# Performance work log

Measured on AMD Instinct MI355X. Metric: run time of the kernel, lower is better.

## Reference

```python
import jax, jax.numpy as jnp
import numpy as np

LOW_THRESH = 0.3
HIGH_THRESH = 0.7
BATCH_SIZE = 256
NUM_POS = BATCH_SIZE // 2   # 128; guaranteed <= total_pos since B2=512 GT boxes are scattered positive
NUM_NEG = BATCH_SIZE - NUM_POS


def _xcycwh_to_x1y1x2y2(b):
    xc, yc, w, h = b[..., 0], b[..., 1], b[..., 2], b[..., 3]
    return jnp.stack([xc - w / 2, yc - h / 2, xc + w / 2, yc + h / 2], axis=-1)


def box_iou(box1, box2):
    # box1: (1, B1, 4), box2: (1, B2, 4) in (xc, yc, w, h) -> iou (1, B1, B2)
    area1 = box1[..., 2] * box1[..., 3]              # (1, B1)
    area2 = box2[..., 2] * box2[..., 3]              # (1, B2)
    c1 = _xcycwh_to_x1y1x2y2(box1)[:, :, None, :]    # (1, B1, 1, 4)
    c2 = _xcycwh_to_x1y1x2y2(box2)[:, None, :, :]    # (1, 1, B2, 4)
    x0 = jnp.maximum(c1[..., 0], c2[..., 0])
    y0 = jnp.maximum(c1[..., 1], c2[..., 1])
    x1 = jnp.minimum(c1[..., 2], c2[..., 2])
    y1 = jnp.minimum(c1[..., 3], c2[..., 3])
    inter = jnp.maximum(x1 - x0, 0.0) * jnp.maximum(y1 - y0, 0.0)  # (1, B1, B2)
    return inter / (area1[:, :, None] + area2[:, None, :] - inter)


def setup_inputs() -> dict:
    key = jax.random.key(0)
    k1, k2, k3, k4 = jax.random.split(key, 4)
    return {
        "input_boxes": jax.random.uniform(k1, (1, 50000, 4), dtype=jnp.float32),
        "target_boxes": jax.random.uniform(k2, (1, 512, 4), dtype=jnp.float32),
        "pos_noise": jax.random.uniform(k3, (50000,), dtype=jnp.float32),
        "neg_noise": jax.random.uniform(k4, (50000,), dtype=jnp.float32),
    }


def reference(input_boxes, target_boxes, pos_noise, neg_noise):
    ious = box_iou(input_boxes, target_boxes)        # (1, B1, B2)
    input_max_iou = jnp.max(ious, axis=2)            # (1, B1) best GT per proposal
    input_idx = jnp.argmax(ious, axis=2)             # (1, B1)
    target_idx = jnp.argmax(ious, axis=1)            # (1, B2) best proposal per GT

    pos_mask = input_max_iou[0] > HIGH_THRESH        # (B1,)
    neg_mask = input_max_iou[0] < LOW_THRESH
    # each GT's best-matching proposal is forced positive (scatter_)
    pos_mask = pos_mask.at[target_idx[0]].set(True)
    neg_mask = neg_mask.at[target_idx[0]].set(False)
    # fallback: if no negatives at all, negatives = complement of positives
    neg_mask = jnp.where(jnp.sum(neg_mask) == 0, ~pos_mask, neg_mask)

    # uniform sampling without replacement == top-k over iid uniform noise restricted to the mask
    pos_scores = jnp.where(pos_mask, pos_noise, -1.0)
    _, pos_input_idx = jax.lax.top_k(pos_scores, NUM_POS)      # (NUM_POS,)
    neg_scores = jnp.where(neg_mask, neg_noise, -1.0)
    _, neg_input_idx = jax.lax.top_k(neg_scores, NUM_NEG)      # (NUM_NEG,)

    pos_target_idx = input_idx[0][pos_input_idx]               # (NUM_POS,)
    return pos_input_idx, pos_target_idx, neg_input_idx
```

## Files before the change

### kernel.cpp

```cpp
#include <hip/hip_runtime.h>
#include <stdint.h>

#pragma clang fp contract(off)

typedef unsigned long long ull;

#define HIGHT 0.7f
#define LOWT  0.3f
#define KSEL  128
#define CAP   2048
#define MAXGT 512
#define TPB   256
#define CHUNK 32
#define TJ    128
#define SMP   132
#define NLAD  7

__device__ __constant__ float LADV[NLAD] = {0.998f, 0.99f, 0.95f, 0.8f, 0.5f, 0.25f, 0.0625f};

__device__ __forceinline__ float iou_pair(float ax0, float ay0, float ax1, float ay1, float aarea,
                                          float bx0, float by0, float bx1, float by1, float barea){
#pragma clang fp contract(off)
  float x0 = fmaxf(ax0, bx0);
  float y0 = fmaxf(ay0, by0);
  float x1 = fminf(ax1, bx1);
  float y1 = fminf(ay1, by1);
  float dx = fmaxf(x1 - x0, 0.0f);
  float dy = fmaxf(y1 - y0, 0.0f);
  float inter = dx * dy;
  float uni = (aarea + barea) - inter;
  return inter / uni;
}

__global__ __launch_bounds__(TPB)
void fused_iou(const float4* __restrict__ boxes, const float4* __restrict__ gts,
               int n1, int n2, int nblk,
               float* __restrict__ max_iou, int* __restrict__ input_idx,
               ull* __restrict__ colpart, int* __restrict__ forced,
               int* __restrict__ cnts_part, int* __restrict__ cnts,
               const float* __restrict__ pn, const float* __restrict__ nn)
{
#pragma clang fp contract(off)
  const int b = blockIdx.x, t = threadIdx.x;

  for (int x = b * TPB + t; x < n1; x += nblk * TPB) forced[x] = 0;
  if (b == 0 && t < 32) cnts[t] = 0;

  __shared__ float4 gc[MAXGT];
  __shared__ float  ga[MAXGT];
  __shared__ float  smat[CHUNK * SMP];
  __shared__ float  sm[CHUNK];

  for (int j = t; j < n2; j += TPB){
    float4 g = gts[j];
    float hw = g.z * 0.5f, hh = g.w * 0.5f;
    gc[j] = make_float4(g.x - hw, g.y - hh, g.x + hw, g.y + hh);
    ga[j] = g.z * g.w;
  }
  __syncthreads();

  const int lo = b * CHUNK;
  int cr = n1 - lo; if (cr > CHUNK) cr = CHUNK; if (cr < 0) cr = 0;

  const int pi = t >> 3, q = t & 7;
  const bool valid = (pi < cr);
  float px0 = 0, py0 = 0, px1 = 0, py1 = 0, pa = 0;
  if (valid){
    float4 pb = boxes[lo + pi];
    float hw = pb.z * 0.5f, hh = pb.w * 0.5f;
    px0 = pb.x - hw; py0 = pb.y - hh; px1 = pb.x + hw; py1 = pb.y + hh;
    pa = pb.z * pb.w;
  }
  float vA = -1.0f, vB = -1.0f; int jA = 0, jB = 0;

  for (int tb = 0; tb < n2; tb += TJ){
    const int tn = min(TJ, n2 - tb);
    if (valid){
      const int jlim = tb + tn;
      int s = 0;
      for (;; s += 2){
        int j0 = tb + q + 8 * s;
        int j1 = j0 + 8;
        if (j1 < jlim){
          float4 g0 = gc[j0]; float a0 = ga[j0];
          float4 g1 = gc[j1]; float a1 = ga[j1];
          float u = iou_pair(px0, py0, px1, py1, pa, g0.x, g0.y, g0.z, g0.w, a0);
          float w = iou_pair(px0, py0, px1, py1, pa, g1.x, g1.y, g1.z, g1.w, a1);
          smat[pi * SMP + (j0 - tb)] = u;
          smat[pi * SMP + (j1 - tb)] = w;
          if (u > vA){ vA = u; jA = j0; }
          if (w > vB){ vB = w; jB = j1; }
        } else {
          if (j0 < jlim){
            float4 g0 = gc[j0]; float a0 = ga[j0];
            float u = iou_pair(px0, py0, px1, py1, pa, g0.x, g0.y, g0.z, g0.w, a0);
            smat[pi * SMP + (j0 - tb)] = u;
            if (u > vA){ vA = u; jA = j0; }
          }
          break;
        }
      }
    }
    __syncthreads();
    {
      const int jloc = t >> 1, half = t & 1;
      if (jloc < tn){
        float cv = -1.0f; int cp = 0;
        const int p0 = half * 16;
        const int p1 = min(p0 + 16, cr);
        for (int p = p0; p < p1; ++p){
          float v = smat[p * SMP + jloc];
          if (v > cv){ cv = v; cp = p; }
        }
        float ov = __shfl_xor(cv, 1, 64);
        int   op = __shfl_xor(cp, 1, 64);
        if (ov > cv || (ov == cv && op < cp)){ cv = ov; cp = op; }
        if (half == 0){
          colpart[(size_t)b * n2 + (tb + jloc)] =
            ((ull)__float_as_uint(cv) << 32) | (ull)(unsigned)~(unsigned)(lo + cp);
        }
      }
    }
    __syncthreads();
  }

  if (vB > vA || (vB == vA && jB < jA)){ vA = vB; jA = jB; }
  #pragma unroll
  for (int m = 1; m <= 4; m <<= 1){
    float ov = __shfl_xor(vA, m, 64);
    int   oj = __shfl_xor(jA, m, 64);
    if (ov > vA || (ov == vA && oj < jA)){ vA = ov; jA = oj; }
  }
  if (valid && q == 0){
    max_iou[lo + pi] = vA;
    input_idx[lo + pi] = jA;
    sm[pi] = vA;
  }
  __syncthreads();

  if (t < 64){
    const bool vld = (t < cr);
    float m = vld ? sm[t] : -1.0f;
    bool pos = vld && (m > HIGHT);
    bool nm  = vld && (m < LOWT);
    bool np  = vld && !(m > HIGHT);
    float sp = pos ? pn[lo + t] : -1.0f;
    float sn = (nm || np) ? nn[lo + t] : -1.0f;
    int c[24];
    c[0] = __popcll(__ballot(pos));
    c[1] = __popcll(__ballot(nm));
    c[2] = __popcll(__ballot(np));
    #pragma unroll
    for (int k = 0; k < NLAD; ++k){
      float L = LADV[k];
      c[3 + k]  = __popcll(__ballot(pos && sp > L));
      c[10 + k] = __popcll(__ballot(nm  && sn > L));
      c[17 + k] = __popcll(__ballot(np  && sn > L));
    }
    if (t == 0){
      #pragma unroll
      for (int k = 0; k < 24; ++k) cnts_part[b * 24 + k] = c[k];
    }
  }
}

__global__ __launch_bounds__(TPB)
void colfix_kernel(const ull* __restrict__ colpart, int n1, int n2, int nblk,
                   const float* __restrict__ max_iou,
                   const float* __restrict__ pn, const float* __restrict__ nn,
                   int* __restrict__ forced, const int* __restrict__ cnts_part,
                   int* __restrict__ cnts)
{
  const int t = threadIdx.x;
  __shared__ ull red[TPB];
  __shared__ int ired[TPB];

  if (blockIdx.x < (unsigned)n2){
    const int jj = blockIdx.x;
    ull m = 0;
    for (int x = t; x < nblk; x += TPB){
      ull v = colpart[(size_t)x * n2 + jj];
      if (v > m) m = v;
    }
    red[t] = m;
    __syncthreads();
    for (int s = TPB >> 1; s > 0; s >>= 1){
      if (t < s && red[t + s] > red[t]) red[t] = red[t + s];
      __syncthreads();
    }
    if (t == 0){
      unsigned idx = ~(unsigned)(red[0] & 0xFFFFFFFFull);
      if (idx < (unsigned)n1){
        int old = atomicExch(&forced[idx], 1);
        if (old == 0){
          float m2 = max_iou[idx];
          if (!(m2 > HIGHT)){
            float sp = pn[idx];
            float sn = nn[idx];
            atomicAdd(&cnts[0], 1);
            atomicAdd(&cnts[2], -1);
            #pragma unroll
            for (int k = 0; k < NLAD; ++k){
              float L = LADV[k];
              if (sp > L) atomicAdd(&cnts[3 + k], 1);
              if (sn > L) atomicAdd(&cnts[17 + k], -1);
            }
            if (m2 < LOWT){
              atomicAdd(&cnts[1], -1);
              #pragma unroll
              for (int k = 0; k < NLAD; ++k)
                if (sn > LADV[k]) atomicAdd(&cnts[10 + k], -1);
            }
          }
        }
      }
    }
  } else {
    const int k = blockIdx.x - n2;
    int s = 0;
    for (int x = t; x < nblk; x += TPB) s += cnts_part[x * 24 + k];
    ired[t] = s;
    __syncthreads();
    for (int st = TPB >> 1; st > 0; st >>= 1){
      if (t < st) ired[t] += ired[t + st];
      __syncthreads();
    }
    if (t == 0 && ired[0]) atomicAdd(&cnts[k], ired[0]);
  }
}

__device__ __forceinline__ float pick_tau(const int* lad, int tot){
  if (tot <= CAP) return -1.0f;
  for (int k = 0; k < NLAD; ++k)
    if (lad[k] >= KSEL) return LADV[k];
  return -1.0f;
}

__global__ __launch_bounds__(TPB)
void collect_kernel(const float* __restrict__ max_iou, const int* __restrict__ forced,
                    const float* __restrict__ pn, const float* __restrict__ nn,
                    int n1, int* __restrict__ cnts, ull* __restrict__ cand)
{
  __shared__ int s_c[24];
  const int t = threadIdx.x;
  if (t < 24) s_c[t] = cnts[t];
  __syncthreads();
  const bool fb = (s_c[1] == 0);
  const int totP = s_c[0];
  const int totN = fb ? s_c[2] : s_c[1];
  const float tauP = pick_tau(&s_c[3], totP);
  const float tauN = pick_tau(fb ? &s_c[17] : &s_c[10], totN);

  const int i = blockIdx.x * TPB + t;
  if (i >= n1) return;
  float m = max_iou[i];
  bool f = forced[i] != 0;
  bool pos = (m > HIGHT) || f;
  if (pos){
    float sc = pn[i];
    if (sc > tauP){
      int p = atomicAdd(&cnts[24], 1);
      if (p < CAP) cand[p] = ((ull)(__float_as_uint(sc) + 1u) << 32) | (ull)(unsigned)~(unsigned)i;
    }
  } else if (totP < KSEL && i < 2 * KSEL){
    int p = atomicAdd(&cnts[24], 1);
    if (p < CAP) cand[p] = (ull)(unsigned)~(unsigned)i;
  }
  bool seln = fb ? (!pos) : ((m < LOWT) && !f);
  if (seln){
    float sc = nn[i];
    if (sc > tauN){
      int p = atomicAdd(&cnts[25], 1);
      if (p < CAP) cand[CAP + p] = ((ull)(__float_as_uint(sc) + 1u) << 32) | (ull)(unsigned)~(unsigned)i;
    }
  } else if (totN < KSEL && i < 2 * KSEL){
    int p = atomicAdd(&cnts[25], 1);
    if (p < CAP) cand[CAP + p] = (ull)(unsigned)~(unsigned)i;
  }
}

__global__ __launch_bounds__(1024)
void select_kernel(const ull* __restrict__ cand, const int* __restrict__ cnts,
                   const int* __restrict__ input_idx, int* __restrict__ out)
{
  const int t = threadIdx.x;
  const bool isPos = (blockIdx.x == 0);
  __shared__ ull keys[CAP];
  int n = cnts[isPos ? 24 : 25]; if (n > CAP) n = CAP;
  for (int x = t; x < n; x += 1024)
    keys[x] = cand[(isPos ? 0 : CAP) + x];
  __syncthreads();
  ull mk[2]; int mr[2]; int ne = 0;
  for (int x = t; x < n; x += 1024){ mk[ne] = keys[x]; mr[ne] = 0; ++ne; }
  for (int o = 0; o < n; ++o){
    ull ko = keys[o];
    if (ne > 0) mr[0] += (ko > mk[0]);
    if (ne > 1) mr[1] += (ko > mk[1]);
  }
  for (int e = 0; e < ne; ++e){
    int r = mr[e];
    if (r < KSEL){
      unsigned idx = ~(unsigned)(mk[e] & 0xFFFFFFFFull);
      if (isPos){ out[r] = (int)idx; out[KSEL + r] = input_idx[idx]; }
      else        out[2 * KSEL + r] = (int)idx;
    }
  }
}

extern "C" void kernel_launch(void* const* d_in, const int* in_sizes, int n_in,
                              void* d_out, int out_size, void* d_ws, size_t ws_size,
                              hipStream_t stream){
  const float4* boxes = (const float4*)d_in[0];
  const float4* gts   = (const float4*)d_in[1];
  const float* pos_noise = (const float*)d_in[2];
  const float* neg_noise = (const float*)d_in[3];
  const int n1 = in_sizes[0] / 4;
  const int n2 = in_sizes[1] / 4;
  int* out = (int*)d_out;

  char* ws = (char*)d_ws;
  size_t off = 0;
  auto carve = [&](size_t bytes) -> char* {
    char* p = ws + off;
    off = (off + bytes + 255) & ~(size_t)255;
    return p;
  };
  const int nblk = (n1 + CHUNK - 1) / CHUNK;
  float* max_iou   = (float*)carve((size_t)n1 * 4);
  int*   input_idx = (int*)  carve((size_t)n1 * 4);
  ull*   colpart   = (ull*)  carve((size_t)nblk * n2 * 8);
  int*   forced    = (int*)  carve((size_t)n1 * 4);
  int*   cnts_part = (int*)  carve((size_t)nblk * 24 * 4);
  int*   cnts      = (int*)  carve(32 * 4);
  ull*   cand      = (ull*)  carve((size_t)2 * CAP * 8);

  const int gb = (n1 + TPB - 1) / TPB;
  fused_iou<<<nblk, TPB, 0, stream>>>(boxes, gts, n1, n2, nblk,
                                      max_iou, input_idx, colpart, forced,
                                      cnts_part, cnts, pos_noise, neg_noise);
  colfix_kernel<<<n2 + 24, TPB, 0, stream>>>(colpart, n1, n2, nblk, max_iou,
                                             pos_noise, neg_noise, forced, cnts_part, cnts);
  collect_kernel<<<gb, TPB, 0, stream>>>(max_iou, forced, pos_noise, neg_noise,
                                         n1, cnts, cand);
  select_kernel<<<2, 1024, 0, stream>>>(cand, cnts, input_idx, out);
}
```

Measured before the change: 137.3 us.

## Replace per-block column partials with global atomicMax and atomic count accumulation

Result: slower. 297.2 us (+116.4%).

```diff
diff --git a/kernel.cpp b/kernel.cpp
--- a/kernel.cpp
+++ b/kernel.cpp
@@ -32,19 +32,27 @@
   return inter / uni;
 }
 
+__global__ __launch_bounds__(256)
+void zero_init(ull* __restrict__ colmax, int* __restrict__ cnts)
+{
+  const int t = threadIdx.x;
+  colmax[t] = 0;
+  colmax[t + 256] = 0;
+  if (t < 32) cnts[t] = 0;
+}
+
 __global__ __launch_bounds__(TPB)
 void fused_iou(const float4* __restrict__ boxes, const float4* __restrict__ gts,
                int n1, int n2, int nblk,
                float* __restrict__ max_iou, int* __restrict__ input_idx,
-               ull* __restrict__ colpart, int* __restrict__ forced,
-               int* __restrict__ cnts_part, int* __restrict__ cnts,
+               ull* __restrict__ colmax, int* __restrict__ forced,
+               int* __restrict__ cnts,
                const float* __restrict__ pn, const float* __restrict__ nn)
 {
 #pragma clang fp contract(off)
   const int b = blockIdx.x, t = threadIdx.x;
 
   for (int x = b * TPB + t; x < n1; x += nblk * TPB) forced[x] = 0;
-  if (b == 0 && t < 32) cnts[t] = 0;
 
   __shared__ float4 gc[MAXGT];
   __shared__ float  ga[MAXGT];
@@ -116,8 +124,8 @@
         int   op = __shfl_xor(cp, 1, 64);
         if (ov > cv || (ov == cv && op < cp)){ cv = ov; cp = op; }
         if (half == 0){
-          colpart[(size_t)b * n2 + (tb + jloc)] =
-            ((ull)__float_as_uint(cv) << 32) | (ull)(unsigned)~(unsigned)(lo + cp);
+          ull key = ((ull)__float_as_uint(cv) << 32) | (ull)(unsigned)~(unsigned)(lo + cp);
+          atomicMax(&colmax[tb + jloc], key);
         }
       }
     }
@@ -159,73 +167,41 @@
     }
     if (t == 0){
       #pragma unroll
-      for (int k = 0; k < 24; ++k) cnts_part[b * 24 + k] = c[k];
-    }
-  }
-}
-
-__global__ __launch_bounds__(TPB)
-void colfix_kernel(const ull* __restrict__ colpart, int n1, int n2, int nblk,
-                   const float* __restrict__ max_iou,
-                   const float* __restrict__ pn, const float* __restrict__ nn,
-                   int* __restrict__ forced, const int* __restrict__ cnts_part,
-                   int* __restrict__ cnts)
+      for (int k = 0; k < 24; ++k) if (c[k]) atomicAdd(&cnts[k], c[k]);
+    }
+  }
+}
+
+__global__ __launch_bounds__(512)
+void forcefix(const ull* __restrict__ colmax, int n1, int n2,
+              const float* __restrict__ max_iou,
+              const float* __restrict__ pn, const float* __restrict__ nn,
+              int* __restrict__ forced, int* __restrict__ cnts)
 {
   const int t = threadIdx.x;
-  __shared__ ull red[TPB];
-  __shared__ int ired[TPB];
-
-  if (blockIdx.x < (unsigned)n2){
-    const int jj = blockIdx.x;
-    ull m = 0;
-    for (int x = t; x < nblk; x += TPB){
-      ull v = colpart[(size_t)x * n2 + jj];
-      if (v > m) m = v;
-    }
-    red[t] = m;
-    __syncthreads();
-    for (int s = TPB >> 1; s > 0; s >>= 1){
-      if (t < s && red[t + s] > red[t]) red[t] = red[t + s];
-      __syncthreads();
-    }
-    if (t == 0){
-      unsigned idx = ~(unsigned)(red[0] & 0xFFFFFFFFull);
-      if (idx < (unsigned)n1){
-        int old = atomicExch(&forced[idx], 1);
-        if (old == 0){
-          float m2 = max_iou[idx];
-          if (!(m2 > HIGHT)){
-            float sp = pn[idx];
-            float sn = nn[idx];
-            atomicAdd(&cnts[0], 1);
-            atomicAdd(&cnts[2], -1);
-            #pragma unroll
-            for (int k = 0; k < NLAD; ++k){
-              float L = LADV[k];
-              if (sp > L) atomicAdd(&cnts[3 + k], 1);
-              if (sn > L) atomicAdd(&cnts[17 + k], -1);
-            }
-            if (m2 < LOWT){
-              atomicAdd(&cnts[1], -1);
-              #pragma unroll
-              for (int k = 0; k < NLAD; ++k)
-                if (sn > LADV[k]) atomicAdd(&cnts[10 + k], -1);
-            }
-          }
-        }
-      }
-    }
-  } else {
-    const int k = blockIdx.x - n2;
-    int s = 0;
-    for (int x = t; x < nblk; x += TPB) s += cnts_part[x * 24 + k];
-    ired[t] = s;
-    __syncthreads();
-    for (int st = TPB >> 1; st > 0; st >>= 1){
-      if (t < st) ired[t] += ired[t + st];
-      __syncthreads();
-    }
-    if (t == 0 && ired[0]) atomicAdd(&cnts[k], ired[0]);
+  if (t >= n2) return;
+  ull key = colmax[t];
+  unsigned idx = ~(unsigned)(key & 0xFFFFFFFFull);
+  if (idx >= (unsigned)n1) return;
+  int old = atomicExch(&forced[idx], 1);
+  if (old != 0) return;
+  float m2 = max_iou[idx];
+  if (m2 > HIGHT) return;
+  float sp = pn[idx];
+  float sn = nn[idx];
+  atomicAdd(&cnts[0], 1);
+  atomicAdd(&cnts[2], -1);
+  #pragma unroll
+  for (int k = 0; k < NLAD; ++k){
+    float L = LADV[k];
+    if (sp > L) atomicAdd(&cnts[3 + k], 1);
+    if (sn > L) atomicAdd(&cnts[17 + k], -1);
+  }
+  if (m2 < LOWT){
+    atomicAdd(&cnts[1], -1);
+    #pragma unroll
+    for (int k = 0; k < NLAD; ++k)
+      if (sn > LADV[k]) atomicAdd(&cnts[10 + k], -1);
   }
 }
 
@@ -328,18 +304,18 @@
   const int nblk = (n1 + CHUNK - 1) / CHUNK;
   float* max_iou   = (float*)carve((size_t)n1 * 4);
   int*   input_idx = (int*)  carve((size_t)n1 * 4);
-  ull*   colpart   = (ull*)  carve((size_t)nblk * n2 * 8);
   int*   forced    = (int*)  carve((size_t)n1 * 4);
-  int*   cnts_part = (int*)  carve((size_t)nblk * 24 * 4);
+  ull*   colmax    = (ull*)  carve((size_t)MAXGT * 8);
   int*   cnts      = (int*)  carve(32 * 4);
   ull*   cand      = (ull*)  carve((size_t)2 * CAP * 8);
 
   const int gb = (n1 + TPB - 1) / TPB;
+  zero_init<<<1, 256, 0, stream>>>(colmax, cnts);
   fused_iou<<<nblk, TPB, 0, stream>>>(boxes, gts, n1, n2, nblk,
-                                      max_iou, input_idx, colpart, forced,
-                                      cnts_part, cnts, pos_noise, neg_noise);
-  colfix_kernel<<<n2 + 24, TPB, 0, stream>>>(colpart, n1, n2, nblk, max_iou,
-                                             pos_noise, neg_noise, forced, cnts_part, cnts);
+                                      max_iou, input_idx, colmax, forced,
+                                      cnts, pos_noise, neg_noise);
+  forcefix<<<1, 512, 0, stream>>>(colmax, n1, n2, max_iou,
+                                  pos_noise, neg_noise, forced, cnts);
   collect_kernel<<<gb, TPB, 0, stream>>>(max_iou, forced, pos_noise, neg_noise,
                                          n1, cnts, cand);
   select_kernel<<<2, 1024, 0, stream>>>(cand, cnts, input_idx, out);
```

## Replace per-column reduction blocks with coalesced grid reduction and last-block fixup

Applied to the files above, without the earlier changes.

Result: slower. 151.5 us (+10.4%).

```diff
diff --git a/kernel.cpp b/kernel.cpp
--- a/kernel.cpp
+++ b/kernel.cpp
@@ -15,6 +15,7 @@
 #define TJ    128
 #define SMP   132
 #define NLAD  7
+#define RB    64
 
 __device__ __constant__ float LADV[NLAD] = {0.998f, 0.99f, 0.95f, 0.8f, 0.5f, 0.25f, 0.0625f};
 
@@ -38,13 +39,17 @@
                float* __restrict__ max_iou, int* __restrict__ input_idx,
                ull* __restrict__ colpart, int* __restrict__ forced,
                int* __restrict__ cnts_part, int* __restrict__ cnts,
+               ull* __restrict__ colmax,
                const float* __restrict__ pn, const float* __restrict__ nn)
 {
 #pragma clang fp contract(off)
   const int b = blockIdx.x, t = threadIdx.x;
 
   for (int x = b * TPB + t; x < n1; x += nblk * TPB) forced[x] = 0;
-  if (b == 0 && t < 32) cnts[t] = 0;
+  if (b == 0){
+    if (t < 32) cnts[t] = 0;
+    for (int x = t; x < n2; x += TPB) colmax[x] = 0;
+  }
 
   __shared__ float4 gc[MAXGT];
   __shared__ float  ga[MAXGT];
@@ -71,34 +76,38 @@
     px0 = pb.x - hw; py0 = pb.y - hh; px1 = pb.x + hw; py1 = pb.y + hh;
     pa = pb.z * pb.w;
   }
-  float vA = -1.0f, vB = -1.0f; int jA = 0, jB = 0;
+  float vA = -1.0f, vB = -1.0f, vC = -1.0f, vD = -1.0f;
+  int jA = 0, jB = 0, jC = 0, jD = 0;
 
   for (int tb = 0; tb < n2; tb += TJ){
     const int tn = min(TJ, n2 - tb);
     if (valid){
       const int jlim = tb + tn;
-      int s = 0;
-      for (;; s += 2){
-        int j0 = tb + q + 8 * s;
-        int j1 = j0 + 8;
-        if (j1 < jlim){
-          float4 g0 = gc[j0]; float a0 = ga[j0];
-          float4 g1 = gc[j1]; float a1 = ga[j1];
-          float u = iou_pair(px0, py0, px1, py1, pa, g0.x, g0.y, g0.z, g0.w, a0);
-          float w = iou_pair(px0, py0, px1, py1, pa, g1.x, g1.y, g1.z, g1.w, a1);
-          smat[pi * SMP + (j0 - tb)] = u;
-          smat[pi * SMP + (j1 - tb)] = w;
-          if (u > vA){ vA = u; jA = j0; }
-          if (w > vB){ vB = w; jB = j1; }
-        } else {
-          if (j0 < jlim){
-            float4 g0 = gc[j0]; float a0 = ga[j0];
-            float u = iou_pair(px0, py0, px1, py1, pa, g0.x, g0.y, g0.z, g0.w, a0);
-            smat[pi * SMP + (j0 - tb)] = u;
-            if (u > vA){ vA = u; jA = j0; }
-          }
-          break;
-        }
+      int j0 = tb + q;
+      for (; j0 + 24 < jlim; j0 += 32){
+        const int ja = j0, jb = j0 + 8, jc = j0 + 16, jd = j0 + 24;
+        float4 gA = gc[ja]; float aA = ga[ja];
+        float4 gB = gc[jb]; float aB = ga[jb];
+        float4 gC = gc[jc]; float aC = ga[jc];
+        float4 gD = gc[jd]; float aD = ga[jd];
+        float u = iou_pair(px0, py0, px1, py1, pa, gA.x, gA.y, gA.z, gA.w, aA);
+        float v = iou_pair(px0, py0, px1, py1, pa, gB.x, gB.y, gB.z, gB.w, aB);
+        float w = iou_pair(px0, py0, px1, py1, pa, gC.x, gC.y, gC.z, gC.w, aC);
+        float x = iou_pair(px0, py0, px1, py1, pa, gD.x, gD.y, gD.z, gD.w, aD);
+        smat[pi * SMP + (ja - tb)] = u;
+        smat[pi * SMP + (jb - tb)] = v;
+        smat[pi * SMP + (jc - tb)] = w;
+        smat[pi * SMP + (jd - tb)] = x;
+        if (u > vA){ vA = u; jA = ja; }
+        if (v > vB){ vB = v; jB = jb; }
+        if (w > vC){ vC = w; jC = jc; }
+        if (x > vD){ vD = x; jD = jd; }
+      }
+      for (; j0 < jlim; j0 += 8){
+        float4 g0 = gc[j0]; float a0 = ga[j0];
+        float u = iou_pair(px0, py0, px1, py1, pa, g0.x, g0.y, g0.z, g0.w, a0);
+        smat[pi * SMP + (j0 - tb)] = u;
+        if (u > vA){ vA = u; jA = j0; }
       }
     }
     __syncthreads();
@@ -125,6 +134,8 @@
   }
 
   if (vB > vA || (vB == vA && jB < jA)){ vA = vB; jA = jB; }
+  if (vC > vA || (vC == vA && jC < jA)){ vA = vC; jA = jC; }
+  if (vD > vA || (vD == vA && jD < jA)){ vA = vD; jA = jD; }
   #pragma unroll
   for (int m = 1; m <= 4; m <<= 1){
     float ov = __shfl_xor(vA, m, 64);
@@ -164,68 +175,63 @@
   }
 }
 
-__global__ __launch_bounds__(TPB)
-void colfix_kernel(const ull* __restrict__ colpart, int n1, int n2, int nblk,
-                   const float* __restrict__ max_iou,
-                   const float* __restrict__ pn, const float* __restrict__ nn,
-                   int* __restrict__ forced, const int* __restrict__ cnts_part,
-                   int* __restrict__ cnts)
+__global__ __launch_bounds__(256)
+void colreduce(const ull* __restrict__ colpart, int n1, int n2, int nblk,
+               const float* __restrict__ max_iou,
+               const float* __restrict__ pn, const float* __restrict__ nn,
+               int* __restrict__ forced, const int* __restrict__ cnts_part,
+               int* __restrict__ cnts, ull* __restrict__ colmax)
 {
-  const int t = threadIdx.x;
-  __shared__ ull red[TPB];
-  __shared__ int ired[TPB];
-
-  if (blockIdx.x < (unsigned)n2){
-    const int jj = blockIdx.x;
+  const int t = threadIdx.x, b = blockIdx.x, nb = gridDim.x;
+
+  for (int j = t; j < n2; j += 256){
     ull m = 0;
-    for (int x = t; x < nblk; x += TPB){
-      ull v = colpart[(size_t)x * n2 + jj];
+    for (int x = b; x < nblk; x += nb){
+      ull v = colpart[(size_t)x * n2 + j];
       if (v > m) m = v;
     }
-    red[t] = m;
-    __syncthreads();
-    for (int s = TPB >> 1; s > 0; s >>= 1){
-      if (t < s && red[t + s] > red[t]) red[t] = red[t + s];
-      __syncthreads();
-    }
-    if (t == 0){
-      unsigned idx = ~(unsigned)(red[0] & 0xFFFFFFFFull);
-      if (idx < (unsigned)n1){
-        int old = atomicExch(&forced[idx], 1);
-        if (old == 0){
-          float m2 = max_iou[idx];
-          if (!(m2 > HIGHT)){
-            float sp = pn[idx];
-            float sn = nn[idx];
-            atomicAdd(&cnts[0], 1);
-            atomicAdd(&cnts[2], -1);
+    if (m) atomicMax(&colmax[j], m);
+  }
+  if (t < 24){
+    int s = 0;
+    for (int x = b; x < nblk; x += nb) s += cnts_part[x * 24 + t];
+    if (s) atomicAdd(&cnts[t], s);
+  }
+
+  __threadfence();
+  __shared__ int islast;
+  if (t == 0) islast = (atomicAdd(&cnts[26], 1) == nb - 1) ? 1 : 0;
+  __syncthreads();
+  if (!islast) return;
+  __threadfence();
+
+  for (int j = t; j < n2; j += 256){
+    ull key = __hip_atomic_load(&colmax[j], __ATOMIC_RELAXED, __HIP_MEMORY_SCOPE_AGENT);
+    unsigned idx = ~(unsigned)(key & 0xFFFFFFFFull);
+    if (idx < (unsigned)n1){
+      int old = atomicExch(&forced[idx], 1);
+      if (old == 0){
+        float m2 = max_iou[idx];
+        if (!(m2 > HIGHT)){
+          float sp = pn[idx];
+          float sn = nn[idx];
+          atomicAdd(&cnts[0], 1);
+          atomicAdd(&cnts[2], -1);
+          #pragma unroll
+          for (int k = 0; k < NLAD; ++k){
+            float L = LADV[k];
+            if (sp > L) atomicAdd(&cnts[3 + k], 1);
+            if (sn > L) atomicAdd(&cnts[17 + k], -1);
+          }
+          if (m2 < LOWT){
+            atomicAdd(&cnts[1], -1);
             #pragma unroll
-            for (int k = 0; k < NLAD; ++k){
-              float L = LADV[k];
-              if (sp > L) atomicAdd(&cnts[3 + k], 1);
-              if (sn > L) atomicAdd(&cnts[17 + k], -1);
-            }
-            if (m2 < LOWT){
-              atomicAdd(&cnts[1], -1);
-              #pragma unroll
-              for (int k = 0; k < NLAD; ++k)
-                if (sn > LADV[k]) atomicAdd(&cnts[10 + k], -1);
-            }
+            for (int k = 0; k < NLAD; ++k)
+              if (sn > LADV[k]) atomicAdd(&cnts[10 + k], -1);
           }
         }
       }
     }
-  } else {
-    const int k = blockIdx.x - n2;
-    int s = 0;
-    for (int x = t; x < nblk; x += TPB) s += cnts_part[x * 24 + k];
-    ired[t] = s;
-    __syncthreads();
-    for (int st = TPB >> 1; st > 0; st >>= 1){
-      if (t < st) ired[t] += ired[t + st];
-      __syncthreads();
-    }
-    if (t == 0 && ired[0]) atomicAdd(&cnts[k], ired[0]);
   }
 }
 
@@ -332,14 +338,15 @@
   int*   forced    = (int*)  carve((size_t)n1 * 4);
   int*   cnts_part = (int*)  carve((size_t)nblk * 24 * 4);
   int*   cnts      = (int*)  carve(32 * 4);
+  ull*   colmax    = (ull*)  carve((size_t)MAXGT * 8);
   ull*   cand      = (ull*)  carve((size_t)2 * CAP * 8);
 
   const int gb = (n1 + TPB - 1) / TPB;
   fused_iou<<<nblk, TPB, 0, stream>>>(boxes, gts, n1, n2, nblk,
                                       max_iou, input_idx, colpart, forced,
-                                      cnts_part, cnts, pos_noise, neg_noise);
-  colfix_kernel<<<n2 + 24, TPB, 0, stream>>>(colpart, n1, n2, nblk, max_iou,
-                                             pos_noise, neg_noise, forced, cnts_part, cnts);
+                                      cnts_part, cnts, colmax, pos_noise, neg_noise);
+  colreduce<<<RB, 256, 0, stream>>>(colpart, n1, n2, nblk, max_iou,
+                                    pos_noise, neg_noise, forced, cnts_part, cnts, colmax);
   collect_kernel<<<gb, TPB, 0, stream>>>(max_iou, forced, pos_noise, neg_noise,
                                          n1, cnts, cand);
   select_kernel<<<2, 1024, 0, stream>>>(cand, cnts, input_idx, out);
```
